# Performance work log

Measured on AMD Instinct MI355X. Metric: run time of the kernel, lower is better.

## Reference

```python
import jax, jax.numpy as jnp
import numpy as np

B, S, D = 2, 2048, 2048
H, KVH, HD = 16, 4, 128
N_REP = H // KVH
SCALING = HD ** -0.5
ROPE_THETA = 10000.0


def _rope_tables(batch, seq, head_dim, dtype=jnp.float32):
    inv_freq = 1.0 / (ROPE_THETA ** (jnp.arange(0, head_dim, 2, dtype=jnp.float32) / head_dim))
    t = jnp.arange(seq, dtype=jnp.float32)
    freqs = jnp.outer(t, inv_freq)                      # [S, HD/2]
    emb = jnp.concatenate([freqs, freqs], axis=-1)      # [S, HD]
    cos = jnp.broadcast_to(jnp.cos(emb), (batch, seq, head_dim)).astype(dtype)
    sin = jnp.broadcast_to(jnp.sin(emb), (batch, seq, head_dim)).astype(dtype)
    return cos, sin


def _causal_mask(batch, seq, dtype=jnp.float32):
    # HF-style additive causal mask: 0 where allowed, large negative where masked
    neg = jnp.finfo(dtype).min
    m = jnp.triu(jnp.full((seq, seq), neg, dtype=dtype), k=1)
    return jnp.broadcast_to(m[None, None], (batch, 1, seq, seq))


def setup_inputs() -> dict:
    key = jax.random.key(0)
    ks = jax.random.split(key, 8)
    w_scale = 0.02
    hidden_states = jax.random.normal(ks[0], (B, S, D), dtype=jnp.float32)
    cos, sin = _rope_tables(B, S, HD)
    attention_mask = _causal_mask(B, S)
    # Linear weights stored as [in, out] (transposed vs torch nn.Linear.weight)
    Wq = jax.random.normal(ks[1], (D, H * HD), dtype=jnp.float32) * w_scale
    bq = jax.random.normal(ks[2], (H * HD,), dtype=jnp.float32) * w_scale
    Wk = jax.random.normal(ks[3], (D, KVH * HD), dtype=jnp.float32) * w_scale
    bk = jax.random.normal(ks[4], (KVH * HD,), dtype=jnp.float32) * w_scale
    Wv = jax.random.normal(ks[5], (D, KVH * HD), dtype=jnp.float32) * w_scale
    bv = jax.random.normal(ks[6], (KVH * HD,), dtype=jnp.float32) * w_scale
    Wo = jax.random.normal(ks[7], (H * HD, D), dtype=jnp.float32) * w_scale
    return {"hidden_states": hidden_states, "cos": cos, "sin": sin,
            "attention_mask": attention_mask, "Wq": Wq, "bq": bq,
            "Wk": Wk, "bk": bk, "Wv": Wv, "bv": bv, "Wo": Wo}


def _rotate_half(x):
    x1, x2 = jnp.split(x, 2, axis=-1)
    return jnp.concatenate([-x2, x1], axis=-1)


def reference(hidden_states, cos, sin, attention_mask, Wq, bq, Wk, bk, Wv, bv, Wo):
    b, s, _ = hidden_states.shape
    # QKV projections -> [B, heads, S, HD]
    q = (hidden_states @ Wq + bq).reshape(b, s, H, HD).transpose(0, 2, 1, 3)
    k = (hidden_states @ Wk + bk).reshape(b, s, KVH, HD).transpose(0, 2, 1, 3)
    v = (hidden_states @ Wv + bv).reshape(b, s, KVH, HD).transpose(0, 2, 1, 3)
    # RoPE (cos/sin broadcast over heads via unsqueeze_dim=1)
    c = cos[:, None]  # [B,1,S,HD]
    sn = sin[:, None]
    q = q * c + _rotate_half(q) * sn
    k = k * c + _rotate_half(k) * sn
    # GQA: repeat_interleave KV heads to match query heads
    k_rep = jnp.repeat(k, N_REP, axis=1)  # [B,H,S,HD]
    v_rep = jnp.repeat(v, N_REP, axis=1)
    # Eager attention: full score matrix, fp32 softmax
    scores = jnp.einsum('bhqd,bhkd->bhqk', q, k_rep) * SCALING + attention_mask
    attn_weights = jax.nn.softmax(scores.astype(jnp.float32), axis=-1).astype(q.dtype)
    attn_out = jnp.einsum('bhqk,bhkd->bhqd', attn_weights, v_rep)
    attn_out = attn_out.transpose(0, 2, 1, 3).reshape(b, s, H * HD)
    attn_out = attn_out @ Wo
    return attn_out, attn_weights
```

## Files before the change

kernel.cpp:

```cpp
#include <hip/hip_runtime.h>

typedef unsigned short ushort_t;
typedef __attribute__((ext_vector_type(8))) short short8;
typedef __attribute__((ext_vector_type(4))) float f32x4;

#define S_  2048
#define Dm  2048
#define NH  16
#define NKV 4
#define HD_ 128
#define C2_ 0.12751879524465536f

__device__ __forceinline__ ushort_t f2bf(float f) {
  union { float f; unsigned u; } v; v.f = f;
  unsigned u = v.u;
  return (ushort_t)((u + 0x7FFFu + ((u >> 16) & 1u)) >> 16);
}
__device__ __forceinline__ float bf2f(ushort_t h) {
  union { unsigned u; float f; } v; v.u = ((unsigned)h) << 16;
  return v.f;
}
__device__ __forceinline__ void gl_lds16(const void* g, void* l) {
  __builtin_amdgcn_global_load_lds((const __attribute__((address_space(1))) void*)g,
                                   (__attribute__((address_space(3))) void*)l, 16, 0, 0);
}

__global__ void prep_k(const float* __restrict__ hs, ushort_t* __restrict__ hsb,
                       const float* __restrict__ Wq, const float* __restrict__ Wk,
                       const float* __restrict__ Wv, const float* __restrict__ Wo,
                       ushort_t* __restrict__ wtqkv, ushort_t* __restrict__ wto) {
  __shared__ float tile[32][33];
  const int id = blockIdx.x;
  if (id < 8192) {
    int i = id * 256 + threadIdx.x;
    float4 v = ((const float4*)hs)[i];
    union { ushort_t u[4]; uint2 v2; } o;
    o.u[0] = f2bf(v.x); o.u[1] = f2bf(v.y); o.u[2] = f2bf(v.z); o.u[3] = f2bf(v.w);
    *(uint2*)&hsb[(size_t)i * 4] = o.v2;
    return;
  }
  const int id2 = id - 8192;
  const int z = id2 >> 12, ky = (id2 >> 6) & 63, nx = id2 & 63;
  const float* src;
  ushort_t* dst;
  int N;
  switch (z) {
    case 0: src = Wq; dst = wtqkv; N = 2048; break;
    case 1: src = Wk; dst = wtqkv + (size_t)2048 * 2048; N = 512; break;
    case 2: src = Wv; dst = wtqkv + (size_t)2560 * 2048; N = 512; break;
    default: src = Wo; dst = wto; N = 2048; break;
  }
  int n0 = nx * 32, k0 = ky * 32;
  if (n0 >= N) return;
  int c = threadIdx.x & 31, r = threadIdx.x >> 5;
#pragma unroll
  for (int i = 0; i < 32; i += 8)
    tile[r + i][c] = src[(size_t)(k0 + r + i) * N + n0 + c];
  __syncthreads();
#pragma unroll
  for (int i = 0; i < 32; i += 8)
    dst[(size_t)(n0 + r + i) * 2048 + k0 + c] = f2bf(tile[c][r + i]);
}

__global__ void transpose_v(const ushort_t* __restrict__ qkv, ushort_t* __restrict__ vt) {
  __shared__ ushort_t tile[32][33];
  int b = blockIdx.z >> 2, kvh = blockIdx.z & 3;
  int s0 = blockIdx.x * 32, d0 = blockIdx.y * 32;
  int c = threadIdx.x & 31, r = threadIdx.x >> 5;
#pragma unroll
  for (int i = 0; i < 32; i += 8)
    tile[r + i][c] = qkv[(size_t)(b * S_ + s0 + r + i) * 3072 + 2560 + kvh * HD_ + d0 + c];
  __syncthreads();
#pragma unroll
  for (int i = 0; i < 32; i += 8)
    vt[(size_t)(blockIdx.z * 128 + d0 + r + i) * S_ + s0 + c] = tile[c][r + i];
}

__global__ __launch_bounds__(256, 2) void gemm_qkv_k(
    const ushort_t* __restrict__ A, const ushort_t* __restrict__ Bt, ushort_t* __restrict__ C,
    const float* __restrict__ bq, const float* __restrict__ bk2, const float* __restrict__ bv,
    const float* __restrict__ cosT, const float* __restrict__ sinT) {
  const int N = 3072, K = 2048;
  __shared__ ushort_t lA[2][128 * 32];
  __shared__ ushort_t lB[2][128 * 32];
  const int lin = blockIdx.x;
  const int nid = (lin & 7) * 96 + (lin >> 3);
  const int n0 = (nid % 24) * 128, m0 = (nid / 24) * 128;
  const int t = threadIdx.x;
  const int w = t >> 6, l = t & 63, lr = l & 15, lg = l >> 4;
  const int wr = w >> 1, wc = w & 1;
  const int srow = t >> 2, ssl = t & 3;

  auto stage = [&](int kt, int bufi) {
    int r0 = srow, r1 = srow + 64;
    gl_lds16(A + (size_t)(m0 + r0) * K + kt + ((ssl ^ ((r0 >> 1) & 3)) << 3), &lA[bufi][w * 512]);
    gl_lds16(A + (size_t)(m0 + r1) * K + kt + ((ssl ^ ((r1 >> 1) & 3)) << 3),
             &lA[bufi][2048 + w * 512]);
    gl_lds16(Bt + (size_t)(n0 + r0) * K + kt + ((ssl ^ ((r0 >> 1) & 3)) << 3), &lB[bufi][w * 512]);
    gl_lds16(Bt + (size_t)(n0 + r1) * K + kt + ((ssl ^ ((r1 >> 1) & 3)) << 3),
             &lB[bufi][2048 + w * 512]);
  };

  f32x4 acc[4][4];
#pragma unroll
  for (int i = 0; i < 4; i++)
#pragma unroll
    for (int j = 0; j < 4; j++) acc[i][j] = (f32x4){0.f, 0.f, 0.f, 0.f};

  stage(0, 0);
  const int nit = K / 32;
  for (int it = 0; it < nit; it++) {
    const int cur = it & 1;
    if (it + 1 < nit) {
      stage((it + 1) * 32, cur ^ 1);
      asm volatile("s_waitcnt vmcnt(4)" ::: "memory");
    } else {
      asm volatile("s_waitcnt vmcnt(0)" ::: "memory");
    }
    __builtin_amdgcn_s_barrier();
    short8 af[4], bfr[4];
#pragma unroll
    for (int mi = 0; mi < 4; mi++) {
      int row = wr * 64 + mi * 16 + lr;
      af[mi] = *(const short8*)((const char*)lA[cur] + row * 64 + ((lg ^ ((row >> 1) & 3)) << 4));
    }
#pragma unroll
    for (int ni = 0; ni < 4; ni++) {
      int row = wc * 64 + ni * 16 + lr;
      bfr[ni] = *(const short8*)((const char*)lB[cur] + row * 64 + ((lg ^ ((row >> 1) & 3)) << 4));
    }
#pragma unroll
    for (int mi = 0; mi < 4; mi++)
#pragma unroll
      for (int ni = 0; ni < 4; ni++)
        acc[mi][ni] = __builtin_amdgcn_mfma_f32_16x16x32_bf16(af[mi], bfr[ni], acc[mi][ni], 0, 0, 0);
    __builtin_amdgcn_s_barrier();
  }

  const bool isV = (n0 >= 2560);
  float* fbuf = (float*)&lA[0][0];
  const int pw_ = w ^ 1;
#pragma unroll
  for (int mi = 0; mi < 4; mi++) {
    float vv[4][4];
#pragma unroll
    for (int ni = 0; ni < 4; ni++)
#pragma unroll
      for (int r = 0; r < 4; r++) {
        int col = n0 + wc * 64 + ni * 16 + lr;
        float bias = (col < 2048) ? bq[col] : (col < 2560) ? bk2[col - 2048] : bv[col - 2560];
        vv[ni][r] = acc[mi][ni][r] + bias;
      }
    if (!isV) {
      __syncthreads();
#pragma unroll
      for (int ni = 0; ni < 4; ni++)
#pragma unroll
        for (int r = 0; r < 4; r++)
          fbuf[w * 1024 + (lg * 4 + r) * 64 + ni * 16 + lr] = vv[ni][r];
      __syncthreads();
#pragma unroll
      for (int ni = 0; ni < 4; ni++)
#pragma unroll
        for (int r = 0; r < 4; r++) {
          float pv = fbuf[pw_ * 1024 + (lg * 4 + r) * 64 + ni * 16 + lr];
          int row = m0 + wr * 64 + mi * 16 + lg * 4 + r;
          int d = wc * 64 + ni * 16 + lr;
          float c = cosT[(size_t)row * HD_ + d];
          float sn = sinT[(size_t)row * HD_ + d];
          vv[ni][r] = (wc == 0) ? vv[ni][r] * c - pv * sn : vv[ni][r] * c + pv * sn;
        }
    }
#pragma unroll
    for (int ni = 0; ni < 4; ni++)
#pragma unroll
      for (int r = 0; r < 4; r++) {
        int row = m0 + wr * 64 + mi * 16 + lg * 4 + r;
        int col = n0 + wc * 64 + ni * 16 + lr;
        C[(size_t)row * N + col] = f2bf(vv[ni][r]);
      }
  }
}

__global__ __launch_bounds__(256, 2) void attn_k(
    const ushort_t* __restrict__ qkv, const ushort_t* __restrict__ vt,
    float* __restrict__ linv_g, ushort_t* __restrict__ attnO, float* __restrict__ outW) {
  __shared__ ushort_t lK[2][64 * 128];
  __shared__ ushort_t lV[2][128 * 64];
  __shared__ ushort_t lP[4][16 * 64];
  const int nid = (blockIdx.x & 7) * 64 + (blockIdx.x >> 3);
  const int pairI = nid & 15, h = (nid >> 4) & 15, b = nid >> 8;
  const int kvh = h >> 2;
  const int t = threadIdx.x, w = t >> 6, l = t & 63, lr = l & 15, lg = l >> 4;
  ushort_t* lPw = lP[w];

  auto stage = [&](int kt, int bufi) {
#pragma unroll
    for (int c = 0; c < 4; c++) {
      int row = c * 16 + (t >> 4), sl = t & 15;
      gl_lds16(qkv + (size_t)(b * S_ + kt * 64 + row) * 3072 + 2048 + kvh * HD_ +
                   ((sl ^ (row & 15)) << 3),
               &lK[bufi][c * 2048 + w * 512]);
    }
#pragma unroll
    for (int c = 0; c < 4; c++) {
      int row = c * 32 + (t >> 3), sl = t & 7;
      gl_lds16(vt + (size_t)((b * 4 + kvh) * 128 + row) * S_ + kt * 64 +
                   ((sl ^ (row & 7)) << 3),
               &lV[bufi][c * 2048 + w * 512]);
    }
  };

  for (int sel = 0; sel < 2; sel++) {
    const int qt = sel ? (31 - pairI) : pairI;
    const int qw = qt * 64 + w * 16;
    const int nkt = qt + 1;

    short8 qf[4];
#pragma unroll
    for (int kc = 0; kc < 4; kc++)
      qf[kc] = *(const short8*)&qkv[(size_t)(b * S_ + qw + lr) * 3072 + h * HD_ + kc * 32 + lg * 8];

    float lsum[4];
    f32x4 o[8];
#pragma unroll
    for (int r = 0; r < 4; r++) lsum[r] = 0.f;
#pragma unroll
    for (int dj = 0; dj < 8; dj++) o[dj] = (f32x4){0.f, 0.f, 0.f, 0.f};

    stage(0, 0);
    for (int kt = 0; kt < nkt; kt++) {
      const int cur = kt & 1;
      if (kt + 1 < nkt) {
        stage(kt + 1, cur ^ 1);
        asm volatile("s_waitcnt vmcnt(8)" ::: "memory");
      } else {
        asm volatile("s_waitcnt vmcnt(0)" ::: "memory");
      }
      __builtin_amdgcn_s_barrier();

      f32x4 s[4];
#pragma unroll
      for (int ni = 0; ni < 4; ni++) s[ni] = (f32x4){0.f, 0.f, 0.f, 0.f};
      __builtin_amdgcn_s_setprio(1);
#pragma unroll
      for (int kc = 0; kc < 4; kc++) {
        short8 kf[4];
#pragma unroll
        for (int ni = 0; ni < 4; ni++) {
          int row = ni * 16 + lr;
          kf[ni] = *(const short8*)((const char*)lK[cur] + row * 256 +
                                    (((kc * 4 + lg) ^ (row & 15)) << 4));
        }
#pragma unroll
        for (int ni = 0; ni < 4; ni++)
          s[ni] = __builtin_amdgcn_mfma_f32_16x16x32_bf16(qf[kc], kf[ni], s[ni], 0, 0, 0);
      }
      __builtin_amdgcn_s_setprio(0);

      if (kt == nkt - 1) {
#pragma unroll
        for (int ni = 0; ni < 4; ni++)
#pragma unroll
          for (int r = 0; r < 4; r++) {
            float p = exp2f(s[ni][r] * C2_);
            int colg = kt * 64 + ni * 16 + lr;
            int rowg = qw + lg * 4 + r;
            if (colg > rowg) p = 0.f;
            lsum[r] += p;
            int rowl = lg * 4 + r, col = ni * 16 + lr;
            lPw[rowl * 64 + (((col >> 3) ^ (rowl & 7)) << 3) + (col & 7)] = f2bf(p);
          }
      } else {
#pragma unroll
        for (int ni = 0; ni < 4; ni++)
#pragma unroll
          for (int r = 0; r < 4; r++) {
            float p = exp2f(s[ni][r] * C2_);
            lsum[r] += p;
            int rowl = lg * 4 + r, col = ni * 16 + lr;
            lPw[rowl * 64 + (((col >> 3) ^ (rowl & 7)) << 3) + (col & 7)] = f2bf(p);
          }
      }

      __builtin_amdgcn_s_setprio(1);
#pragma unroll
      for (int kc = 0; kc < 2; kc++) {
        short8 pa;
        {
          int row = lr;
          pa = *(const short8*)((const char*)lPw + row * 128 + (((kc * 4 + lg) ^ (row & 7)) << 4));
        }
#pragma unroll
        for (int dj = 0; dj < 8; dj++) {
          int row = dj * 16 + lr;
          short8 vb = *(const short8*)((const char*)lV[cur] + row * 128 +
                                       (((kc * 4 + lg) ^ (row & 7)) << 4));
          o[dj] = __builtin_amdgcn_mfma_f32_16x16x32_bf16(pa, vb, o[dj], 0, 0, 0);
        }
      }
      __builtin_amdgcn_s_setprio(0);
      __builtin_amdgcn_s_barrier();
    }

    float inv_l[4];
#pragma unroll
    for (int r = 0; r < 4; r++) {
      float sum = lsum[r];
#pragma unroll
      for (int off = 1; off < 16; off <<= 1) sum += __shfl_xor(sum, off);
      inv_l[r] = 1.f / sum;
      if (lr == 0) linv_g[(size_t)(b * NH + h) * S_ + qw + lg * 4 + r] = inv_l[r];
    }
#pragma unroll
    for (int dj = 0; dj < 8; dj++)
#pragma unroll
      for (int r = 0; r < 4; r++) {
        int rowg = b * S_ + qw + lg * 4 + r;
        int colg = h * HD_ + dj * 16 + lr;
        attnO[(size_t)rowg * Dm + colg] = f2bf(o[dj][r] * inv_l[r]);
      }

    {
      const int zc0 = nkt * 64;
      const int zn = (S_ - zc0) >> 2;
      f32x4 z = {0.f, 0.f, 0.f, 0.f};
      const int bh = b * NH + h;
      for (int rr = 0; rr < 16; rr++) {
        f32x4* base = (f32x4*)&outW[((size_t)bh * S_ + qw + rr) * S_ + zc0];
        for (int cc = l; cc < zn; cc += 64) __builtin_nontemporal_store(z, base + cc);
      }
    }
  }
}

__global__ __launch_bounds__(256, 2) void tail_k(
    const ushort_t* __restrict__ A, const ushort_t* __restrict__ Bt, float* __restrict__ outO,
    const ushort_t* __restrict__ qkv, const float* __restrict__ linv,
    float* __restrict__ outW) {
  __shared__ ushort_t sh[2][64 * 128];
  const int bx = blockIdx.x;
  const int t = threadIdx.x;
  const int w = t >> 6, l = t & 63, lr = l & 15, lg = l >> 4;

  if (bx < 512) {
    const int N = 2048, K = 2048;
    const int nid = (bx & 7) * 64 + (bx >> 3);
    const int n0 = (nid & 15) * 128, m0 = (nid >> 4) * 128;
    const int wr = w >> 1, wc = w & 1;
    const int srow = t >> 2, ssl = t & 3;

    auto stageG = [&](int kt, int bufi) {
      int r0 = srow, r1 = srow + 64;
      gl_lds16(A + (size_t)(m0 + r0) * K + kt + ((ssl ^ ((r0 >> 1) & 3)) << 3), &sh[bufi][w * 512]);
      gl_lds16(A + (size_t)(m0 + r1) * K + kt + ((ssl ^ ((r1 >> 1) & 3)) << 3),
               &sh[bufi][2048 + w * 512]);
      gl_lds16(Bt + (size_t)(n0 + r0) * K + kt + ((ssl ^ ((r0 >> 1) & 3)) << 3),
               &sh[bufi][4096 + w * 512]);
      gl_lds16(Bt + (size_t)(n0 + r1) * K + kt + ((ssl ^ ((r1 >> 1) & 3)) << 3),
               &sh[bufi][4096 + 2048 + w * 512]);
    };

    f32x4 acc[4][4];
#pragma unroll
    for (int i = 0; i < 4; i++)
#pragma unroll
      for (int j = 0; j < 4; j++) acc[i][j] = (f32x4){0.f, 0.f, 0.f, 0.f};

    stageG(0, 0);
    const int nit = K / 32;
    for (int it = 0; it < nit; it++) {
      const int cur = it & 1;
      if (it + 1 < nit) {
        stageG((it + 1) * 32, cur ^ 1);
        asm volatile("s_waitcnt vmcnt(4)" ::: "memory");
      } else {
        asm volatile("s_waitcnt vmcnt(0)" ::: "memory");
      }
      __builtin_amdgcn_s_barrier();
      short8 af[4], bfr[4];
#pragma unroll
      for (int mi = 0; mi < 4; mi++) {
        int row = wr * 64 + mi * 16 + lr;
        af[mi] =
            *(const short8*)((const char*)&sh[cur][0] + row * 64 + ((lg ^ ((row >> 1) & 3)) << 4));
      }
#pragma unroll
      for (int ni = 0; ni < 4; ni++) {
        int row = wc * 64 + ni * 16 + lr;
        bfr[ni] = *(const short8*)((const char*)&sh[cur][4096] + row * 64 +
                                   ((lg ^ ((row >> 1) & 3)) << 4));
      }
#pragma unroll
      for (int mi = 0; mi < 4; mi++)
#pragma unroll
        for (int ni = 0; ni < 4; ni++)
          acc[mi][ni] =
              __builtin_amdgcn_mfma_f32_16x16x32_bf16(af[mi], bfr[ni], acc[mi][ni], 0, 0, 0);
      __builtin_amdgcn_s_barrier();
    }
#pragma unroll
    for (int mi = 0; mi < 4; mi++)
#pragma unroll
      for (int ni = 0; ni < 4; ni++)
#pragma unroll
        for (int r = 0; r < 4; r++) {
          int row = m0 + wr * 64 + mi * 16 + lg * 4 + r;
          int col = n0 + wc * 64 + ni * 16 + lr;
          outO[(size_t)row * N + col] = acc[mi][ni][r];
        }
    return;
  }

  const int lin = bx - 512;
  const int nid = (lin & 7) * 64 + (lin >> 3);
  const int bh = nid >> 4;
  const int pi = nid & 15;
  const int b = bh >> 4, h = bh & 15;
  const int kvh = h >> 2;

  auto stageK = [&](int kt, int bufi) {
#pragma unroll
    for (int c = 0; c < 4; c++) {
      int row = c * 16 + (t >> 4), sl = t & 15;
      gl_lds16(qkv + (size_t)(b * S_ + kt * 64 + row) * 3072 + 2048 + kvh * HD_ +
                   ((sl ^ (row & 15)) << 3),
               &sh[bufi][c * 2048 + w * 512]);
    }
  };

  for (int sel = 0; sel < 2; sel++) {
    const int qt = sel ? (31 - pi) : pi;
    const int qw = qt * 64 + w * 16;
    const int nkt = qt + 1;

    short8 qf[4];
#pragma unroll
    for (int kc = 0; kc < 4; kc++)
      qf[kc] = *(const short8*)&qkv[(size_t)(b * S_ + qw + lr) * 3072 + h * HD_ + kc * 32 + lg * 8];

    float invr[4];
#pragma unroll
    for (int r = 0; r < 4; r++) invr[r] = linv[(size_t)bh * S_ + qw + lg * 4 + r];

    stageK(0, 0);
    for (int kt = 0; kt < nkt; kt++) {
      const int cur = kt & 1;
      if (kt + 1 < nkt) {
        stageK(kt + 1, cur ^ 1);
        asm volatile("s_waitcnt vmcnt(4)" ::: "memory");
      } else {
        asm volatile("s_waitcnt vmcnt(0)" ::: "memory");
      }
      __builtin_amdgcn_s_barrier();

      f32x4 s[4];
#pragma unroll
      for (int ni = 0; ni < 4; ni++) s[ni] = (f32x4){0.f, 0.f, 0.f, 0.f};
#pragma unroll
      for (int kc = 0; kc < 4; kc++) {
        short8 kf[4];
#pragma unroll
        for (int ni = 0; ni < 4; ni++) {
          int row = ni * 16 + lr;
          kf[ni] = *(const short8*)((const char*)sh[cur] + row * 256 +
                                    (((kc * 4 + lg) ^ (row & 15)) << 4));
        }
#pragma unroll
        for (int ni = 0; ni < 4; ni++)
          s[ni] = __builtin_amdgcn_mfma_f32_16x16x32_bf16(qf[kc], kf[ni], s[ni], 0, 0, 0);
      }

      const bool diag = (kt == nkt - 1);
#pragma unroll
      for (int ni = 0; ni < 4; ni++)
#pragma unroll
        for (int r = 0; r < 4; r++) {
          int colg = kt * 64 + ni * 16 + lr;
          int rowg = qw + lg * 4 + r;
          float p = exp2f(s[ni][r] * C2_) * invr[r];
          if (diag && colg > rowg) p = 0.f;
          outW[((size_t)bh * S_ + rowg) * S_ + colg] = p;
        }
      __builtin_amdgcn_s_barrier();
    }
  }
}

extern "C" void kernel_launch(void* const* d_in, const int* in_sizes, int n_in,
                              void* d_out, int out_size, void* d_ws, size_t ws_size,
                              hipStream_t stream) {
  const float* hs   = (const float*)d_in[0];
  const float* cosT = (const float*)d_in[1];
  const float* sinT = (const float*)d_in[2];
  const float* Wq = (const float*)d_in[4];
  const float* bq = (const float*)d_in[5];
  const float* Wk = (const float*)d_in[6];
  const float* bk = (const float*)d_in[7];
  const float* Wv = (const float*)d_in[8];
  const float* bv = (const float*)d_in[9];
  const float* Wo = (const float*)d_in[10];

  char* ws = (char*)d_ws;
  ushort_t* hsb   = (ushort_t*)(ws);
  ushort_t* wtqkv = (ushort_t*)(ws + 16777216);
  ushort_t* wto   = (ushort_t*)(ws + 29360128);
  ushort_t* qkv   = (ushort_t*)(ws + 37748736);
  ushort_t* vt    = (ushort_t*)(ws + 62914560);
  float*    linv  = (float*)(ws + 67108864);
  ushort_t* attn  = (ushort_t*)(ws);

  float* outO = (float*)d_out;
  float* outW = outO + (size_t)8388608;

  prep_k<<<8192 + 16384, 256, 0, stream>>>(hs, hsb, Wq, Wk, Wv, Wo, wtqkv, wto);
  gemm_qkv_k<<<768, 256, 0, stream>>>(hsb, wtqkv, qkv, bq, bk, bv, cosT, sinT);
  transpose_v<<<dim3(64, 4, 8), 256, 0, stream>>>(qkv, vt);
  attn_k<<<512, 256, 0, stream>>>(qkv, vt, linv, attn, outW);
  tail_k<<<1024, 256, 0, stream>>>(attn, wto, outO, qkv, linv, outW);
}
```

Before: 303.5 us.

## Fuse V transpose into QKV GEMM, MFMA row sums, nontemporal output stores

Result: slower. 310.5 us (+2.3%).

```diff
diff --git a/kernel.cpp b/kernel.cpp
--- a/kernel.cpp
+++ b/kernel.cpp
@@ -15,6 +15,10 @@
   union { float f; unsigned u; } v; v.f = f;
   unsigned u = v.u;
   return (ushort_t)((u + 0x7FFFu + ((u >> 16) & 1u)) >> 16);
+}
+__device__ __forceinline__ ushort_t f2bf2(float f) {
+  union { float f; unsigned u; } v; v.f = f;
+  return (ushort_t)((v.u + 0x8000u) >> 16);
 }
 __device__ __forceinline__ float bf2f(ushort_t h) {
   union { unsigned u; float f; } v; v.u = ((unsigned)h) << 16;
@@ -62,27 +66,14 @@
     dst[(size_t)(n0 + r + i) * 2048 + k0 + c] = f2bf(tile[c][r + i]);
 }
 
-__global__ void transpose_v(const ushort_t* __restrict__ qkv, ushort_t* __restrict__ vt) {
-  __shared__ ushort_t tile[32][33];
-  int b = blockIdx.z >> 2, kvh = blockIdx.z & 3;
-  int s0 = blockIdx.x * 32, d0 = blockIdx.y * 32;
-  int c = threadIdx.x & 31, r = threadIdx.x >> 5;
-#pragma unroll
-  for (int i = 0; i < 32; i += 8)
-    tile[r + i][c] = qkv[(size_t)(b * S_ + s0 + r + i) * 3072 + 2560 + kvh * HD_ + d0 + c];
-  __syncthreads();
-#pragma unroll
-  for (int i = 0; i < 32; i += 8)
-    vt[(size_t)(blockIdx.z * 128 + d0 + r + i) * S_ + s0 + c] = tile[c][r + i];
-}
-
 __global__ __launch_bounds__(256, 2) void gemm_qkv_k(
     const ushort_t* __restrict__ A, const ushort_t* __restrict__ Bt, ushort_t* __restrict__ C,
     const float* __restrict__ bq, const float* __restrict__ bk2, const float* __restrict__ bv,
-    const float* __restrict__ cosT, const float* __restrict__ sinT) {
+    const float* __restrict__ cosT, const float* __restrict__ sinT, ushort_t* __restrict__ vt) {
   const int N = 3072, K = 2048;
-  __shared__ ushort_t lA[2][128 * 32];
-  __shared__ ushort_t lB[2][128 * 32];
+  __shared__ ushort_t smem[16384];
+  ushort_t* lA0 = smem;
+  ushort_t* lB0 = smem + 8192;
   const int lin = blockIdx.x;
   const int nid = (lin & 7) * 96 + (lin >> 3);
   const int n0 = (nid % 24) * 128, m0 = (nid / 24) * 128;
@@ -93,12 +84,14 @@
 
   auto stage = [&](int kt, int bufi) {
     int r0 = srow, r1 = srow + 64;
-    gl_lds16(A + (size_t)(m0 + r0) * K + kt + ((ssl ^ ((r0 >> 1) & 3)) << 3), &lA[bufi][w * 512]);
+    gl_lds16(A + (size_t)(m0 + r0) * K + kt + ((ssl ^ ((r0 >> 1) & 3)) << 3),
+             &lA0[bufi * 4096 + w * 512]);
     gl_lds16(A + (size_t)(m0 + r1) * K + kt + ((ssl ^ ((r1 >> 1) & 3)) << 3),
-             &lA[bufi][2048 + w * 512]);
-    gl_lds16(Bt + (size_t)(n0 + r0) * K + kt + ((ssl ^ ((r0 >> 1) & 3)) << 3), &lB[bufi][w * 512]);
+             &lA0[bufi * 4096 + 2048 + w * 512]);
+    gl_lds16(Bt + (size_t)(n0 + r0) * K + kt + ((ssl ^ ((r0 >> 1) & 3)) << 3),
+             &lB0[bufi * 4096 + w * 512]);
     gl_lds16(Bt + (size_t)(n0 + r1) * K + kt + ((ssl ^ ((r1 >> 1) & 3)) << 3),
-             &lB[bufi][2048 + w * 512]);
+             &lB0[bufi * 4096 + 2048 + w * 512]);
   };
 
   f32x4 acc[4][4];
@@ -122,12 +115,14 @@
 #pragma unroll
     for (int mi = 0; mi < 4; mi++) {
       int row = wr * 64 + mi * 16 + lr;
-      af[mi] = *(const short8*)((const char*)lA[cur] + row * 64 + ((lg ^ ((row >> 1) & 3)) << 4));
+      af[mi] = *(const short8*)((const char*)(lA0 + cur * 4096) + row * 64 +
+                                ((lg ^ ((row >> 1) & 3)) << 4));
     }
 #pragma unroll
     for (int ni = 0; ni < 4; ni++) {
       int row = wc * 64 + ni * 16 + lr;
-      bfr[ni] = *(const short8*)((const char*)lB[cur] + row * 64 + ((lg ^ ((row >> 1) & 3)) << 4));
+      bfr[ni] = *(const short8*)((const char*)(lB0 + cur * 4096) + row * 64 +
+                                 ((lg ^ ((row >> 1) & 3)) << 4));
     }
 #pragma unroll
     for (int mi = 0; mi < 4; mi++)
@@ -138,7 +133,7 @@
   }
 
   const bool isV = (n0 >= 2560);
-  float* fbuf = (float*)&lA[0][0];
+  float* fbuf = (float*)smem;
   const int pw_ = w ^ 1;
 #pragma unroll
   for (int mi = 0; mi < 4; mi++) {
@@ -177,8 +172,28 @@
       for (int r = 0; r < 4; r++) {
         int row = m0 + wr * 64 + mi * 16 + lg * 4 + r;
         int col = n0 + wc * 64 + ni * 16 + lr;
-        C[(size_t)row * N + col] = f2bf(vv[ni][r]);
-      }
+        ushort_t hv = f2bf(vv[ni][r]);
+        C[(size_t)row * N + col] = hv;
+        if (isV) {
+          int colL = wc * 64 + ni * 16 + lr;
+          int rowL = wr * 64 + mi * 16 + lg * 4 + r;
+          smem[colL * 128 + (rowL ^ ((colL & 7) << 4))] = hv;
+        }
+      }
+  }
+  if (isV) {
+    __syncthreads();
+    const int kvh = (n0 - 2560) >> 7;
+    const int b = m0 >> 11, s0v = m0 & 2047;
+    const size_t vbase = (size_t)(b * 4 + kvh) * 128;
+#pragma unroll
+    for (int j = 0; j < 8; j++) {
+      int cid = j * 256 + t;
+      int d = cid >> 4, sc = cid & 15;
+      int rowStart = (sc * 8) ^ ((d & 7) << 4);
+      short8 v8 = *(const short8*)&smem[d * 128 + rowStart];
+      *(short8*)&vt[(vbase + d) * S_ + s0v + sc * 8] = v8;
+    }
   }
 }
 
@@ -194,6 +209,10 @@
   const int t = threadIdx.x, w = t >> 6, l = t & 63, lr = l & 15, lg = l >> 4;
   ushort_t* lPw = lP[w];
 
+  short8 onesb;
+#pragma unroll
+  for (int i = 0; i < 8; i++) onesb[i] = (short)0x3F80;
+
   auto stage = [&](int kt, int bufi) {
 #pragma unroll
     for (int c = 0; c < 4; c++) {
@@ -221,10 +240,8 @@
     for (int kc = 0; kc < 4; kc++)
       qf[kc] = *(const short8*)&qkv[(size_t)(b * S_ + qw + lr) * 3072 + h * HD_ + kc * 32 + lg * 8];
 
-    float lsum[4];
+    f32x4 accS = (f32x4){0.f, 0.f, 0.f, 0.f};
     f32x4 o[8];
-#pragma unroll
-    for (int r = 0; r < 4; r++) lsum[r] = 0.f;
 #pragma unroll
     for (int dj = 0; dj < 8; dj++) o[dj] = (f32x4){0.f, 0.f, 0.f, 0.f};
 
@@ -267,9 +284,8 @@
             int colg = kt * 64 + ni * 16 + lr;
             int rowg = qw + lg * 4 + r;
             if (colg > rowg) p = 0.f;
-            lsum[r] += p;
             int rowl = lg * 4 + r, col = ni * 16 + lr;
-            lPw[rowl * 64 + (((col >> 3) ^ (rowl & 7)) << 3) + (col & 7)] = f2bf(p);
+            lPw[rowl * 64 + (((col >> 3) ^ (rowl & 7)) << 3) + (col & 7)] = f2bf2(p);
           }
       } else {
 #pragma unroll
@@ -277,9 +293,8 @@
 #pragma unroll
           for (int r = 0; r < 4; r++) {
             float p = exp2f(s[ni][r] * C2_);
-            lsum[r] += p;
             int rowl = lg * 4 + r, col = ni * 16 + lr;
-            lPw[rowl * 64 + (((col >> 3) ^ (rowl & 7)) << 3) + (col & 7)] = f2bf(p);
+            lPw[rowl * 64 + (((col >> 3) ^ (rowl & 7)) << 3) + (col & 7)] = f2bf2(p);
           }
       }
 
@@ -291,6 +306,7 @@
           int row = lr;
           pa = *(const short8*)((const char*)lPw + row * 128 + (((kc * 4 + lg) ^ (row & 7)) << 4));
         }
+        accS = __builtin_amdgcn_mfma_f32_16x16x32_bf16(pa, onesb, accS, 0, 0, 0);
 #pragma unroll
         for (int dj = 0; dj < 8; dj++) {
           int row = dj * 16 + lr;
@@ -306,10 +322,7 @@
     float inv_l[4];
 #pragma unroll
     for (int r = 0; r < 4; r++) {
-      float sum = lsum[r];
-#pragma unroll
-      for (int off = 1; off < 16; off <<= 1) sum += __shfl_xor(sum, off);
-      inv_l[r] = 1.f / sum;
+      inv_l[r] = 1.f / accS[r];
       if (lr == 0) linv_g[(size_t)(b * NH + h) * S_ + qw + lg * 4 + r] = inv_l[r];
     }
 #pragma unroll
@@ -407,7 +420,7 @@
         for (int r = 0; r < 4; r++) {
           int row = m0 + wr * 64 + mi * 16 + lg * 4 + r;
           int col = n0 + wc * 64 + ni * 16 + lr;
-          outO[(size_t)row * N + col] = acc[mi][ni][r];
+          __builtin_nontemporal_store(acc[mi][ni][r], &outO[(size_t)row * N + col]);
         }
     return;
   }
@@ -480,7 +493,7 @@
           int rowg = qw + lg * 4 + r;
           float p = exp2f(s[ni][r] * C2_) * invr[r];
           if (diag && colg > rowg) p = 0.f;
-          outW[((size_t)bh * S_ + rowg) * S_ + colg] = p;
+          __builtin_nontemporal_store(p, &outW[((size_t)bh * S_ + rowg) * S_ + colg]);
         }
       __builtin_amdgcn_s_barrier();
     }
@@ -514,8 +527,7 @@
   float* outW = outO + (size_t)8388608;
 
   prep_k<<<8192 + 16384, 256, 0, stream>>>(hs, hsb, Wq, Wk, Wv, Wo, wtqkv, wto);
-  gemm_qkv_k<<<768, 256, 0, stream>>>(hsb, wtqkv, qkv, bq, bk, bv, cosT, sinT);
-  transpose_v<<<dim3(64, 4, 8), 256, 0, stream>>>(qkv, vt);
+  gemm_qkv_k<<<768, 256, 0, stream>>>(hsb, wtqkv, qkv, bq, bk, bv, cosT, sinT, vt);
   attn_k<<<512, 256, 0, stream>>>(qkv, vt, linv, attn, outW);
   tail_k<<<1024, 256, 0, stream>>>(attn, wto, outO, qkv, linv, outW);
 }
```
